# Optimization experiments

Measured on AMD Instinct MI355X. Metric: run time of the kernel, lower is better.

The kernel has to match this reference:

```python
import jax, jax.numpy as jnp
import numpy as np

T = 2048
HIDDEN = 4096
NH = 32        # query heads
NKV = 8        # kv heads
G = NH // NKV  # GQA group size
D = 128        # head_dim (== v_head_dim)
ROPE_BASE = 1000000.0


def setup_inputs() -> dict:
    key = jax.random.key(0)
    ks = jax.random.split(key, 8)
    s = 0.02
    return {
        "positions": jnp.arange(T, dtype=jnp.int32),
        "hidden_states": jax.random.normal(ks[0], (T, HIDDEN), dtype=jnp.float32),
        "Wq": jax.random.normal(ks[1], (HIDDEN, NH * D), dtype=jnp.float32) * s,
        "bq": jnp.zeros((NH * D,), dtype=jnp.float32),
        "Wk": jax.random.normal(ks[2], (HIDDEN, NKV * D), dtype=jnp.float32) * s,
        "bk": jnp.zeros((NKV * D,), dtype=jnp.float32),
        "Wv": jax.random.normal(ks[3], (HIDDEN, NKV * D), dtype=jnp.float32) * s,
        "bv": jnp.zeros((NKV * D,), dtype=jnp.float32),
        "Wo": jax.random.normal(ks[4], (NH * D, HIDDEN), dtype=jnp.float32) * s,
    }


def _rope(positions, x):
    # neox-style rotary, full rotary_dim = D
    half = D // 2
    inv_freq = 1.0 / (ROPE_BASE ** (jnp.arange(0, half, dtype=jnp.float32) / half))
    freqs = positions.astype(jnp.float32)[:, None] * inv_freq[None, :]  # [T, half]
    cos = jnp.cos(freqs)[:, None, :]  # [T, 1, half]
    sin = jnp.sin(freqs)[:, None, :]
    x1, x2 = x[..., :half], x[..., half:]
    return jnp.concatenate([x1 * cos - x2 * sin, x2 * cos + x1 * sin], axis=-1)


def reference(positions, hidden_states, Wq, bq, Wk, bk, Wv, bv, Wo):
    q = (hidden_states @ Wq + bq).reshape(T, NH, D)
    k = (hidden_states @ Wk + bk).reshape(T, NKV, D)
    v = (hidden_states @ Wv + bv).reshape(T, NKV, D)
    q = _rope(positions, q)
    k = _rope(positions, k)

    scale = D ** -0.5
    qg = q.reshape(T, NKV, G, D)
    # scores: [NKV, G, T(query), S(key)]
    scores = jnp.einsum("tkgd,skd->kgts", qg, k) * scale
    causal = positions[:, None] >= positions[None, :]  # [T, S]
    scores = jnp.where(causal[None, None, :, :], scores, jnp.finfo(scores.dtype).min)
    probs = jax.nn.softmax(scores, axis=-1)
    attn = jnp.einsum("kgts,skd->tkgd", probs, v).reshape(T, NH * D)

    output = attn @ Wo
    kv_fused = jnp.stack([k, v], axis=0)  # [2, T, NKV, D]
    return output, kv_fused
```

## Files before the change

### kernel.cpp

```cpp
#include <hip/hip_runtime.h>
#include <stdint.h>

#define T_SEQ 2048
#define HIDDEN_DIM 4096
#define NH 32
#define NKV 8
#define HD 128
#define QKV_N 6144

typedef unsigned short u16;
typedef __attribute__((__ext_vector_type__(8))) __bf16 bf16x8;
typedef __attribute__((__ext_vector_type__(4))) float f32x4;

__device__ __forceinline__ float exp2_fast(float x) {
    return __builtin_amdgcn_exp2f(x);
}

__device__ __forceinline__ u16 f2bf(float f) {
    union { float f; unsigned u; } x; x.f = f;
    unsigned u = x.u;
    unsigned r = u + 0x7FFFu + ((u >> 16) & 1u);
    return (u16)(r >> 16);
}
__device__ __forceinline__ float bf2f(u16 h) {
    union { unsigned u; float f; } x; x.u = ((unsigned)h) << 16;
    return x.f;
}

__device__ __forceinline__ void gl_lds16(const u16* g, u16* l) {
    __builtin_amdgcn_global_load_lds((__attribute__((address_space(1))) void*)g,
                                     (__attribute__((address_space(3))) void*)l,
                                     16, 0, 0);
}

__global__ __launch_bounds__(256) void cast_f32_bf16(const float* __restrict__ in,
                                                     u16* __restrict__ out, int n4) {
    int i = blockIdx.x * 256 + threadIdx.x;
    if (i < n4) {
        float4 v = ((const float4*)in)[i];
        uint2 o;
        o.x = (unsigned)f2bf(v.x) | ((unsigned)f2bf(v.y) << 16);
        o.y = (unsigned)f2bf(v.z) | ((unsigned)f2bf(v.w) << 16);
        ((uint2*)out)[i] = o;
    }
}

__global__ __launch_bounds__(256) void transpose_cast(const float* __restrict__ W,
                                                      u16* __restrict__ Wt, int R, int C) {
    __shared__ float tile[32][33];
    int c0 = blockIdx.x * 32, r0 = blockIdx.y * 32;
    int tx = threadIdx.x & 31;
    int ty = threadIdx.x >> 5;
#pragma unroll
    for (int i = 0; i < 32; i += 8)
        tile[ty + i][tx] = W[(size_t)(r0 + ty + i) * C + c0 + tx];
    __syncthreads();
#pragma unroll
    for (int i = 0; i < 32; i += 8)
        Wt[(size_t)(c0 + ty + i) * R + r0 + tx] = f2bf(tile[tx][ty + i]);
}

__global__ __launch_bounds__(256) void concat_bias(const float* __restrict__ bq,
                                                   const float* __restrict__ bk,
                                                   const float* __restrict__ bv,
                                                   float* __restrict__ out) {
    int i = blockIdx.x * 256 + threadIdx.x;
    if (i < 4096) out[i] = bq[i];
    else if (i < 5120) out[i] = bk[i - 4096];
    else if (i < 6144) out[i] = bv[i - 5120];
}

template <int BF16_OUT, int HAS_BIAS>
__global__ __launch_bounds__(256) void gemm_bt(const u16* __restrict__ A,
                                               const u16* __restrict__ Bt,
                                               const float* __restrict__ bias,
                                               void* __restrict__ Cv,
                                               int M, int N, int K) {
    __shared__ alignas(16) u16 As[128 * 32];
    __shared__ alignas(16) u16 Bs[128 * 32];
    const int tid = threadIdx.x;
    const int wave = tid >> 6;
    const int lane = tid & 63;
    const int l15 = lane & 15;
    const int quad = lane >> 4;
    const int m0 = blockIdx.y * 128;
    const int n0 = blockIdx.x * 128;
    const int wm = (wave >> 1) * 64;
    const int wn = (wave & 1) * 64;

    f32x4 acc[4][4] = {};

    const u16* Ag = A + (size_t)(m0 + wave * 32 + (lane >> 2)) * K + (lane & 3) * 8;
    const u16* Bg = Bt + (size_t)(n0 + wave * 32 + (lane >> 2)) * K + (lane & 3) * 8;
    u16* Al = &As[wave * 32 * 32];
    u16* Bl = &Bs[wave * 32 * 32];

    for (int k0 = 0; k0 < K; k0 += 32) {
        __syncthreads();
        gl_lds16(Ag + k0, Al);
        gl_lds16(Ag + k0 + (size_t)16 * K, Al + 16 * 32);
        gl_lds16(Bg + k0, Bl);
        gl_lds16(Bg + k0 + (size_t)16 * K, Bl + 16 * 32);
        __syncthreads();
        bf16x8 af[4], bfr[4];
#pragma unroll
        for (int i = 0; i < 4; ++i)
            af[i] = *(const bf16x8*)&As[(wm + i * 16 + l15) * 32 + quad * 8];
#pragma unroll
        for (int i = 0; i < 4; ++i)
            bfr[i] = *(const bf16x8*)&Bs[(wn + i * 16 + l15) * 32 + quad * 8];
#pragma unroll
        for (int i = 0; i < 4; ++i)
#pragma unroll
            for (int j = 0; j < 4; ++j)
                acc[i][j] = __builtin_amdgcn_mfma_f32_16x16x32_bf16(af[i], bfr[j], acc[i][j], 0, 0, 0);
    }

#pragma unroll
    for (int i = 0; i < 4; ++i)
#pragma unroll
        for (int j = 0; j < 4; ++j)
#pragma unroll
            for (int r = 0; r < 4; ++r) {
                int row = m0 + wm + i * 16 + quad * 4 + r;
                int col = n0 + wn + j * 16 + l15;
                float v = acc[i][j][r];
                if (HAS_BIAS) v += bias[col];
                if (BF16_OUT) ((u16*)Cv)[(size_t)row * N + col] = f2bf(v);
                else ((float*)Cv)[(size_t)row * N + col] = v;
            }
}

__global__ __launch_bounds__(256) void rope_kernel(const int* __restrict__ positions,
                                                   const u16* __restrict__ qkv,
                                                   u16* __restrict__ qh,
                                                   u16* __restrict__ kh,
                                                   u16* __restrict__ vt,
                                                   float* __restrict__ kv_out) {
    const int t = blockIdx.x;
    const float pos = (float)positions[t];
    const size_t rowbase = (size_t)t * QKV_N;
    const float nlog = -13.815510557964274f / 64.f;
    const float KZ = 0.08838834764831845f * 1.4426950408889634f;
    for (int col = threadIdx.x; col < QKV_N; col += 256) {
        if (col < 4096) {
            int hh = col >> 7, d = col & 127, j = d & 63;
            float ang = pos * __expf((float)j * nlog);
            float cs = cosf(ang), sn = sinf(ang);
            size_t base = rowbase + (size_t)(col & ~127);
            float x1 = bf2f(qkv[base + j]);
            float x2 = bf2f(qkv[base + 64 + j]);
            float v = (d < 64) ? (x1 * cs - x2 * sn) : (x2 * cs + x1 * sn);
            qh[((size_t)hh * T_SEQ + t) * HD + d] = f2bf(v * KZ);
        } else if (col < 5120) {
            int lc = col - 4096, hh = lc >> 7, d = lc & 127, j = d & 63;
            float ang = pos * __expf((float)j * nlog);
            float cs = cosf(ang), sn = sinf(ang);
            size_t base = rowbase + 4096 + (size_t)hh * 128;
            float x1 = bf2f(qkv[base + j]);
            float x2 = bf2f(qkv[base + 64 + j]);
            float v = (d < 64) ? (x1 * cs - x2 * sn) : (x2 * cs + x1 * sn);
            kh[((size_t)hh * T_SEQ + t) * HD + d] = f2bf(v);
            kv_out[((size_t)t * NKV + hh) * HD + d] = v;
        } else {
            int lc = col - 5120, hh = lc >> 7, d = lc & 127;
            float v = bf2f(qkv[rowbase + 5120 + (size_t)hh * 128 + d]);
            vt[((size_t)hh * HD + d) * T_SEQ + t] = f2bf(v);
            kv_out[(((size_t)T_SEQ + t) * NKV + hh) * HD + d] = v;
        }
    }
}

#define KS_STRIDE 136
#define VS_STRIDE 72
#define PS_STRIDE 72

__global__ __launch_bounds__(256) void attn_kernel(const u16* __restrict__ Qh,
                                                   const u16* __restrict__ Kh,
                                                   const u16* __restrict__ Vt,
                                                   u16* __restrict__ attn_out) {
    __shared__ alignas(16) u16 Ks[64 * KS_STRIDE];
    __shared__ alignas(16) u16 Vs[128 * VS_STRIDE];
    __shared__ alignas(16) u16 Ps[4][32 * PS_STRIDE];

    const int h = blockIdx.y;
    const int qb = (gridDim.x - 1) - blockIdx.x;
    const int tid = threadIdx.x;
    const int wave = tid >> 6;
    const int lane = tid & 63;
    const int l15 = lane & 15;
    const int quad = lane >> 4;
    const int kvh = h >> 2;
    const int wrow0 = qb * 128 + wave * 32;

    const u16* Qp = Qh + ((size_t)h * T_SEQ + wrow0) * HD;
    const u16* Kp = Kh + (size_t)kvh * T_SEQ * HD;
    const u16* Vp = Vt + (size_t)kvh * HD * T_SEQ;

    bf16x8 aQ[2][4];
#pragma unroll
    for (int i = 0; i < 2; ++i)
#pragma unroll
        for (int kb = 0; kb < 4; ++kb)
            aQ[i][kb] = *(const bf16x8*)&Qp[(size_t)(i * 16 + l15) * HD + kb * 32 + quad * 8];

    bf16x8 ones;
#pragma unroll
    for (int z = 0; z < 8; ++z) ones[z] = (__bf16)1.0f;

    f32x4 acc[2][8] = {};
    f32x4 accl[2] = {};

    const int n_tiles = 2 * qb + 2;

    const int krow = tid >> 4;
    const int kcol = (tid & 15) * 8;
    const int vrow = tid >> 3;
    const int vcol = (tid & 7) * 8;

#pragma unroll 1
    for (int t = 0; t < n_tiles; ++t) {
        const int s0 = t * 64;
        __syncthreads();
#pragma unroll
        for (int rep = 0; rep < 4; ++rep) {
            int r = krow + rep * 16;
            *(uint4*)&Ks[r * KS_STRIDE + kcol] =
                *(const uint4*)&Kp[(size_t)(s0 + r) * HD + kcol];
        }
#pragma unroll
        for (int rep = 0; rep < 4; ++rep) {
            int d = vrow + rep * 32;
            *(uint4*)&Vs[d * VS_STRIDE + vcol] =
                *(const uint4*)&Vp[(size_t)d * T_SEQ + s0 + vcol];
        }
        __syncthreads();

        if (s0 <= wrow0 + 31) {
            f32x4 sc[2][4];
#pragma unroll
            for (int j = 0; j < 4; ++j) {
                f32x4 sa = {}, sb = {};
#pragma unroll
                for (int kb = 0; kb < 4; ++kb) {
                    bf16x8 bK = *(const bf16x8*)&Ks[(j * 16 + l15) * KS_STRIDE + kb * 32 + quad * 8];
                    sa = __builtin_amdgcn_mfma_f32_16x16x32_bf16(aQ[0][kb], bK, sa, 0, 0, 0);
                    sb = __builtin_amdgcn_mfma_f32_16x16x32_bf16(aQ[1][kb], bK, sb, 0, 0, 0);
                }
                sc[0][j] = sa;
                sc[1][j] = sb;
            }
#pragma unroll
            for (int i = 0; i < 2; ++i)
#pragma unroll
                for (int r = 0; r < 4; ++r) {
                    int t_idx = wrow0 + i * 16 + quad * 4 + r;
#pragma unroll
                    for (int j = 0; j < 4; ++j) {
                        int s_idx = s0 + j * 16 + l15;
                        float z = (s_idx > t_idx) ? -1e30f : sc[i][j][r];
                        float p = exp2_fast(z);
                        Ps[wave][(i * 16 + quad * 4 + r) * PS_STRIDE + j * 16 + l15] = f2bf(p);
                    }
                }
            bf16x8 aP[2][2];
#pragma unroll
            for (int i = 0; i < 2; ++i)
#pragma unroll
                for (int k2 = 0; k2 < 2; ++k2)
                    aP[i][k2] = *(const bf16x8*)&Ps[wave][(i * 16 + l15) * PS_STRIDE + k2 * 32 + quad * 8];
#pragma unroll
            for (int o = 0; o < 8; ++o) {
                bf16x8 bV0 = *(const bf16x8*)&Vs[(o * 16 + l15) * VS_STRIDE + quad * 8];
                bf16x8 bV1 = *(const bf16x8*)&Vs[(o * 16 + l15) * VS_STRIDE + 32 + quad * 8];
#pragma unroll
                for (int i = 0; i < 2; ++i) {
                    acc[i][o] = __builtin_amdgcn_mfma_f32_16x16x32_bf16(aP[i][0], bV0, acc[i][o], 0, 0, 0);
                    acc[i][o] = __builtin_amdgcn_mfma_f32_16x16x32_bf16(aP[i][1], bV1, acc[i][o], 0, 0, 0);
                }
            }
#pragma unroll
            for (int i = 0; i < 2; ++i) {
                accl[i] = __builtin_amdgcn_mfma_f32_16x16x32_bf16(aP[i][0], ones, accl[i], 0, 0, 0);
                accl[i] = __builtin_amdgcn_mfma_f32_16x16x32_bf16(aP[i][1], ones, accl[i], 0, 0, 0);
            }
        }
    }

#pragma unroll
    for (int i = 0; i < 2; ++i)
#pragma unroll
        for (int r = 0; r < 4; ++r) {
            float inv = 1.f / accl[i][r];
            int t_idx = wrow0 + i * 16 + quad * 4 + r;
#pragma unroll
            for (int o = 0; o < 8; ++o)
                attn_out[(size_t)t_idx * (NH * HD) + h * HD + o * 16 + l15] =
                    f2bf(acc[i][o][r] * inv);
        }
}

extern "C" void kernel_launch(void* const* d_in, const int* in_sizes, int n_in,
                              void* d_out, int out_size, void* d_ws, size_t ws_size,
                              hipStream_t stream) {
    const int* positions = (const int*)d_in[0];
    const float* hidden = (const float*)d_in[1];
    const float* Wq = (const float*)d_in[2];
    const float* bq = (const float*)d_in[3];
    const float* Wk = (const float*)d_in[4];
    const float* bk = (const float*)d_in[5];
    const float* Wv = (const float*)d_in[6];
    const float* bv = (const float*)d_in[7];
    const float* Wo = (const float*)d_in[8];

    char* ws = (char*)d_ws;
    u16* hs_bf   = (u16*)(ws + 0);
    u16* attnbuf = (u16*)(ws + 0);
    u16* wqkvT   = (u16*)(ws + 16777216);
    u16* woT     = (u16*)(ws + 16777216);
    u16* qkvbuf  = (u16*)(ws + 67108864);
    u16* qbuf    = (u16*)(ws + 92274688);
    u16* kbuf    = (u16*)(ws + 109051904);
    u16* vtbuf   = (u16*)(ws + 113246208);
    float* biasb = (float*)(ws + 117440512);

    float* out0 = (float*)d_out;
    float* kvout = out0 + (size_t)T_SEQ * HIDDEN_DIM;

    cast_f32_bf16<<<dim3((T_SEQ * HIDDEN_DIM / 4 + 255) / 256), dim3(256), 0, stream>>>(
        hidden, hs_bf, T_SEQ * HIDDEN_DIM / 4);
    transpose_cast<<<dim3(128, 128), dim3(256), 0, stream>>>(Wq, wqkvT, HIDDEN_DIM, 4096);
    transpose_cast<<<dim3(32, 128), dim3(256), 0, stream>>>(Wk, wqkvT + (size_t)4096 * HIDDEN_DIM, HIDDEN_DIM, 1024);
    transpose_cast<<<dim3(32, 128), dim3(256), 0, stream>>>(Wv, wqkvT + (size_t)5120 * HIDDEN_DIM, HIDDEN_DIM, 1024);
    concat_bias<<<dim3(24), dim3(256), 0, stream>>>(bq, bk, bv, biasb);

    gemm_bt<1, 1><<<dim3(QKV_N / 128, T_SEQ / 128), dim3(256), 0, stream>>>(
        hs_bf, wqkvT, biasb, qkvbuf, T_SEQ, QKV_N, HIDDEN_DIM);

    transpose_cast<<<dim3(128, 128), dim3(256), 0, stream>>>(Wo, woT, NH * HD, HIDDEN_DIM);

    rope_kernel<<<dim3(T_SEQ), dim3(256), 0, stream>>>(positions, qkvbuf, qbuf, kbuf, vtbuf, kvout);

    attn_kernel<<<dim3(16, NH), dim3(256), 0, stream>>>(qbuf, kbuf, vtbuf, attnbuf);

    gemm_bt<0, 0><<<dim3(HIDDEN_DIM / 128, T_SEQ / 128), dim3(256), 0, stream>>>(
        attnbuf, woT, nullptr, out0, T_SEQ, HIDDEN_DIM, NH * HD);
}
```

Measured before the change: 580.2 us.

## Use 256x256-tile 4-stage pipelined GEMM for QKV projection

Adds a new 512-thread GEMM kernel with 256x256 output tiles, a 4-slot LDS ring buffer fed by direct global-to-LDS loads, XOR-swizzled LDS layout, setprio around MFMA bursts, and a blockIdx swizzle for L2 locality. It replaces the 128x128 QKV projection GEMM. The aim is more data reuse per tile and overlap of loads with MFMA. The cost is much higher register and LDS pressure (128 KB of LDS per block) and fewer blocks (192) on a large CU count, which may leave parts of the GPU underused.

```diff
diff --git a/kernel.cpp b/kernel.cpp
--- a/kernel.cpp
+++ b/kernel.cpp
@@ -32,6 +32,13 @@
                                      (__attribute__((address_space(3))) void*)l,
                                      16, 0, 0);
 }
+
+#define BAR()                                  \
+    {                                          \
+        asm volatile("" ::: "memory");         \
+        __builtin_amdgcn_s_barrier();          \
+        asm volatile("" ::: "memory");         \
+    }
 
 __global__ __launch_bounds__(256) void cast_f32_bf16(const float* __restrict__ in,
                                                      u16* __restrict__ out, int n4) {
@@ -129,6 +136,131 @@
                 if (BF16_OUT) ((u16*)Cv)[(size_t)row * N + col] = f2bf(v);
                 else ((float*)Cv)[(size_t)row * N + col] = v;
             }
+}
+
+#define KSTEP(S, SLOT, STG, VMW)                                                            \
+    {                                                                                       \
+        bf16x8 bf0_[4], af_[4];                                                             \
+        _Pragma("unroll") for (int n = 0; n < 4; ++n)                                       \
+            bf0_[n] = *(const bf16x8*)&Bs[SLOT][boff[n]];                                   \
+        _Pragma("unroll") for (int m = 0; m < 4; ++m)                                       \
+            af_[m] = *(const bf16x8*)&As[SLOT][aoff[m]];                                    \
+        if (STG) {                                                                          \
+            gl_lds16(Ast + (size_t)((S) + 3) * 32, &As[((SLOT) + 3) & 3][ldsS0]);           \
+            gl_lds16(Ast + (size_t)((S) + 3) * 32 + rowK128, &As[((SLOT) + 3) & 3][ldsS1]); \
+        }                                                                                   \
+        BAR();                                                                              \
+        __builtin_amdgcn_s_setprio(1);                                                      \
+        _Pragma("unroll") for (int m = 0; m < 4; ++m)                                       \
+            _Pragma("unroll") for (int n = 0; n < 4; ++n)                                   \
+                acc[m][n] = __builtin_amdgcn_mfma_f32_16x16x32_bf16(af_[m], bf0_[n],        \
+                                                                    acc[m][n], 0, 0, 0);    \
+        __builtin_amdgcn_s_setprio(0);                                                      \
+        BAR();                                                                              \
+        _Pragma("unroll") for (int m = 0; m < 4; ++m)                                       \
+            af_[m] = *(const bf16x8*)&As[SLOT][aoff[4 + m]];                                \
+        if (STG) {                                                                          \
+            gl_lds16(Bst + (size_t)((S) + 3) * 32, &Bs[((SLOT) + 3) & 3][ldsS0]);           \
+            gl_lds16(Bst + (size_t)((S) + 3) * 32 + rowK128, &Bs[((SLOT) + 3) & 3][ldsS1]); \
+        }                                                                                   \
+        BAR();                                                                              \
+        __builtin_amdgcn_s_setprio(1);                                                      \
+        _Pragma("unroll") for (int m = 0; m < 4; ++m)                                       \
+            _Pragma("unroll") for (int n = 0; n < 4; ++n)                                   \
+                acc[4 + m][n] = __builtin_amdgcn_mfma_f32_16x16x32_bf16(af_[m], bf0_[n],    \
+                                                                        acc[4 + m][n],      \
+                                                                        0, 0, 0);           \
+        __builtin_amdgcn_s_setprio(0);                                                      \
+        asm volatile("s_waitcnt vmcnt(" #VMW ")" ::: "memory");                             \
+        BAR();                                                                              \
+    }
+
+template <int BF16_OUT, int HAS_BIAS>
+__global__ __launch_bounds__(512, 2) void gemm256(const u16* __restrict__ A,
+                                                  const u16* __restrict__ Bt,
+                                                  const float* __restrict__ bias,
+                                                  void* __restrict__ Cv,
+                                                  int M, int N, int K) {
+    __shared__ alignas(16) u16 As[4][256 * 32];
+    __shared__ alignas(16) u16 Bs[4][256 * 32];
+    const int tid = threadIdx.x;
+    const int wave = tid >> 6;
+    const int lane = tid & 63;
+    const int l15 = lane & 15;
+    const int quad = lane >> 4;
+    const int wr = wave >> 2;
+    const int wc = wave & 3;
+
+    const int nbx = N >> 8;
+    const int q8 = (int)gridDim.x >> 3;
+    const int wg = blockIdx.x;
+    const int swz = (wg & 7) * q8 + (wg >> 3);
+    const int m0 = (swz / nbx) * 256;
+    const int n0 = (swz % nbx) * 256;
+
+    const int srow = tid >> 2;
+    const int schunk = (tid & 3) ^ ((tid >> 3) & 3);
+    const u16* Ast = A + (size_t)(m0 + srow) * K + schunk * 8;
+    const u16* Bst = Bt + (size_t)(n0 + srow) * K + schunk * 8;
+    const size_t rowK128 = (size_t)128 * K;
+    const int ldsS0 = wave * 512;
+    const int ldsS1 = 4096 + wave * 512;
+
+    int aoff[8], boff[4];
+#pragma unroll
+    for (int m = 0; m < 8; ++m) {
+        int row = wr * 128 + m * 16 + l15;
+        aoff[m] = row * 32 + ((quad ^ ((row >> 1) & 3)) << 3);
+    }
+#pragma unroll
+    for (int n = 0; n < 4; ++n) {
+        int row = wc * 64 + n * 16 + l15;
+        boff[n] = row * 32 + ((quad ^ ((row >> 1) & 3)) << 3);
+    }
+
+    f32x4 acc[8][4] = {};
+    const int NS = K >> 5;
+
+#pragma unroll
+    for (int s = 0; s < 3; ++s) {
+        gl_lds16(Ast + (size_t)s * 32, &As[s][ldsS0]);
+        gl_lds16(Ast + (size_t)s * 32 + rowK128, &As[s][ldsS1]);
+        gl_lds16(Bst + (size_t)s * 32, &Bs[s][ldsS0]);
+        gl_lds16(Bst + (size_t)s * 32 + rowK128, &Bs[s][ldsS1]);
+    }
+    asm volatile("s_waitcnt vmcnt(8)" ::: "memory");
+    BAR();
+
+#pragma unroll 1
+    for (int s = 0; s < NS - 4; s += 4) {
+        KSTEP(s, 0, 1, 4)
+        KSTEP(s + 1, 1, 1, 4)
+        KSTEP(s + 2, 2, 1, 4)
+        KSTEP(s + 3, 3, 1, 4)
+    }
+    {
+        const int s = NS - 4;
+        KSTEP(s, 0, 1, 4)
+        KSTEP(s + 1, 1, 0, 4)
+        KSTEP(s + 2, 2, 0, 0)
+        KSTEP(s + 3, 3, 0, 0)
+    }
+
+#pragma unroll
+    for (int m = 0; m < 8; ++m) {
+        const int row = m0 + wr * 128 + m * 16 + quad * 4;
+#pragma unroll
+        for (int n = 0; n < 4; ++n) {
+            const int col = n0 + wc * 64 + n * 16 + l15;
+            float b = HAS_BIAS ? bias[col] : 0.f;
+#pragma unroll
+            for (int r = 0; r < 4; ++r) {
+                float v = acc[m][n][r] + b;
+                if (BF16_OUT) ((u16*)Cv)[(size_t)(row + r) * N + col] = f2bf(v);
+                else ((float*)Cv)[(size_t)(row + r) * N + col] = v;
+            }
+        }
+    }
 }
 
 __global__ __launch_bounds__(256) void rope_kernel(const int* __restrict__ positions,
@@ -334,7 +466,7 @@
     transpose_cast<<<dim3(32, 128), dim3(256), 0, stream>>>(Wv, wqkvT + (size_t)5120 * HIDDEN_DIM, HIDDEN_DIM, 1024);
     concat_bias<<<dim3(24), dim3(256), 0, stream>>>(bq, bk, bv, biasb);
 
-    gemm_bt<1, 1><<<dim3(QKV_N / 128, T_SEQ / 128), dim3(256), 0, stream>>>(
+    gemm256<1, 1><<<dim3((T_SEQ / 256) * (QKV_N / 256)), dim3(512), 0, stream>>>(
         hs_bf, wqkvT, biasb, qkvbuf, T_SEQ, QKV_N, HIDDEN_DIM);
 
     transpose_cast<<<dim3(128, 128), dim3(256), 0, stream>>>(Wo, woT, NH * HD, HIDDEN_DIM);
```

Measured after the change: 564.2 us. 1.03x faster.

## Replace GEMMs with 4-stage pipelined, swizzled 512-thread MFMA kernel; zigzag attention schedule

Applied to the files above, without the earlier changes.

Replaces the single-buffered 128x128 GEMM with a templated kernel that uses a 4-slot LDS ring filled by global_load_lds. It double-buffers register fragments, waits on explicit vmcnt counts, swizzles LDS chunks against bank conflicts, remaps workgroups for L2 locality, and raises MFMA priority with s_setprio. The QKV and output projections get larger 256x192 and 128x256 tiles with 8 waves. Attention blocks are reordered in a zigzag pattern that alternates by head to balance causal work. The aim is to hide global-load latency and raise MFMA utilisation, at the cost of more LDS and registers per block and hand-tuned wait counts that must match the number of outstanding loads.

```diff
diff --git a/kernel.cpp b/kernel.cpp
--- a/kernel.cpp
+++ b/kernel.cpp
@@ -31,6 +31,22 @@
     __builtin_amdgcn_global_load_lds((__attribute__((address_space(1))) void*)g,
                                      (__attribute__((address_space(3))) void*)l,
                                      16, 0, 0);
+}
+
+#define BAR()                                  \
+    {                                          \
+        asm volatile("" ::: "memory");         \
+        __builtin_amdgcn_s_barrier();          \
+        asm volatile("" ::: "memory");         \
+    }
+
+template <int N>
+__device__ __forceinline__ void vmwait() {
+    if constexpr (N == 0) asm volatile("s_waitcnt vmcnt(0)" ::: "memory");
+    else if constexpr (N == 3) asm volatile("s_waitcnt vmcnt(3)" ::: "memory");
+    else if constexpr (N == 4) asm volatile("s_waitcnt vmcnt(4)" ::: "memory");
+    else if constexpr (N == 6) asm volatile("s_waitcnt vmcnt(6)" ::: "memory");
+    else if constexpr (N == 8) asm volatile("s_waitcnt vmcnt(8)" ::: "memory");
 }
 
 __global__ __launch_bounds__(256) void cast_f32_bf16(const float* __restrict__ in,
@@ -70,65 +86,128 @@
     else if (i < 6144) out[i] = bv[i - 5120];
 }
 
-template <int BF16_OUT, int HAS_BIAS>
-__global__ __launch_bounds__(256) void gemm_bt(const u16* __restrict__ A,
-                                               const u16* __restrict__ Bt,
-                                               const float* __restrict__ bias,
-                                               void* __restrict__ Cv,
-                                               int M, int N, int K) {
-    __shared__ alignas(16) u16 As[128 * 32];
-    __shared__ alignas(16) u16 Bs[128 * 32];
+#define STAGE(SL, S)                                                                         \
+    {                                                                                        \
+        const size_t ko_ = (size_t)(S) * 32;                                                 \
+        _Pragma("unroll") for (int c_ = 0; c_ < ACALLS; ++c_)                                \
+            gl_lds16(Ast + ko_ + (size_t)(c_ * 128) * K, &As[SL][c_ * 4096 + wave * 512]);   \
+        _Pragma("unroll") for (int c_ = 0; c_ < BFULL; ++c_)                                 \
+            gl_lds16(Bst + ko_ + (size_t)(c_ * 128) * K, &Bs[SL][c_ * 4096 + wave * 512]);   \
+        if (BHALF) gl_lds16(BstH + ko_, &Bs[SL][BFULL * 4096 + (wave & 3) * 512]);           \
+    }
+
+#define REGION(SLOT, NSLOT, CA, CB, NA, NB, RN)                                              \
+    {                                                                                        \
+        if (RN) {                                                                            \
+            _Pragma("unroll") for (int n_ = 0; n_ < NF; ++n_)                                \
+                NB[n_] = *(const bf16x8*)&Bs[NSLOT][boff[n_]];                               \
+            _Pragma("unroll") for (int m_ = 0; m_ < MF; ++m_)                                \
+                NA[m_] = *(const bf16x8*)&As[NSLOT][aoff[m_]];                               \
+        }                                                                                    \
+        __builtin_amdgcn_s_setprio(1);                                                       \
+        _Pragma("unroll") for (int m_ = 0; m_ < MF; ++m_)                                    \
+            _Pragma("unroll") for (int n_ = 0; n_ < NF; ++n_)                                \
+                acc[m_][n_] = __builtin_amdgcn_mfma_f32_16x16x32_bf16(CA[m_], CB[n_],        \
+                                                                      acc[m_][n_], 0, 0, 0); \
+        __builtin_amdgcn_s_setprio(0);                                                       \
+    }
+
+#define KSTEP(S, SLOT, STG, VMW, RN, CA, CB, NA, NB)          \
+    {                                                         \
+        if (STG) STAGE((((SLOT) + 3) & 3), (S) + 3)           \
+        vmwait<VMW>();                                        \
+        BAR();                                                \
+        REGION(SLOT, (((SLOT) + 1) & 3), CA, CB, NA, NB, RN)  \
+        BAR();                                                \
+    }
+
+template <int MF, int NF, int ACALLS, int BFULL, int BHALF, int BF16_OUT, int HAS_BIAS>
+__global__ __launch_bounds__(512, 2) void gemm_ph(const u16* __restrict__ A,
+                                                  const u16* __restrict__ Bt,
+                                                  const float* __restrict__ bias,
+                                                  void* __restrict__ Cv,
+                                                  int M, int N, int K) {
+    constexpr int BM = MF * 32;
+    constexpr int BN = NF * 64;
+    constexpr int LPS = ACALLS + BFULL + BHALF;
+    __shared__ alignas(16) u16 As[4][BM * 32];
+    __shared__ alignas(16) u16 Bs[4][BN * 32];
     const int tid = threadIdx.x;
     const int wave = tid >> 6;
     const int lane = tid & 63;
     const int l15 = lane & 15;
     const int quad = lane >> 4;
-    const int m0 = blockIdx.y * 128;
-    const int n0 = blockIdx.x * 128;
-    const int wm = (wave >> 1) * 64;
-    const int wn = (wave & 1) * 64;
-
-    f32x4 acc[4][4] = {};
-
-    const u16* Ag = A + (size_t)(m0 + wave * 32 + (lane >> 2)) * K + (lane & 3) * 8;
-    const u16* Bg = Bt + (size_t)(n0 + wave * 32 + (lane >> 2)) * K + (lane & 3) * 8;
-    u16* Al = &As[wave * 32 * 32];
-    u16* Bl = &Bs[wave * 32 * 32];
-
-    for (int k0 = 0; k0 < K; k0 += 32) {
-        __syncthreads();
-        gl_lds16(Ag + k0, Al);
-        gl_lds16(Ag + k0 + (size_t)16 * K, Al + 16 * 32);
-        gl_lds16(Bg + k0, Bl);
-        gl_lds16(Bg + k0 + (size_t)16 * K, Bl + 16 * 32);
-        __syncthreads();
-        bf16x8 af[4], bfr[4];
-#pragma unroll
-        for (int i = 0; i < 4; ++i)
-            af[i] = *(const bf16x8*)&As[(wm + i * 16 + l15) * 32 + quad * 8];
-#pragma unroll
-        for (int i = 0; i < 4; ++i)
-            bfr[i] = *(const bf16x8*)&Bs[(wn + i * 16 + l15) * 32 + quad * 8];
-#pragma unroll
-        for (int i = 0; i < 4; ++i)
-#pragma unroll
-            for (int j = 0; j < 4; ++j)
-                acc[i][j] = __builtin_amdgcn_mfma_f32_16x16x32_bf16(af[i], bfr[j], acc[i][j], 0, 0, 0);
-    }
-
-#pragma unroll
-    for (int i = 0; i < 4; ++i)
-#pragma unroll
-        for (int j = 0; j < 4; ++j)
+    const int wr = wave >> 2;
+    const int wc = wave & 3;
+
+    const int nbn = N / BN;
+    const int q8 = (int)gridDim.x >> 3;
+    const int wg = blockIdx.x;
+    const int swz = (wg & 7) * q8 + (wg >> 3);
+    const int m0 = (swz / nbn) * BM;
+    const int n0 = (swz % nbn) * BN;
+
+    const int srow = tid >> 2;
+    const int schunk = (tid & 3) ^ ((tid >> 3) & 3);
+    const u16* Ast = A + (size_t)(m0 + srow) * K + schunk * 8;
+    const u16* Bst = Bt + (size_t)(n0 + srow) * K + schunk * 8;
+    const int srowH = (tid & 255) >> 2;
+    const u16* BstH = Bt + (size_t)(n0 + BFULL * 128 + srowH) * K + schunk * 8;
+
+    int aoff[MF], boff[NF];
+#pragma unroll
+    for (int m = 0; m < MF; ++m) {
+        int row = wr * (MF * 16) + m * 16 + l15;
+        aoff[m] = row * 32 + ((quad ^ ((row >> 1) & 3)) << 3);
+    }
+#pragma unroll
+    for (int n = 0; n < NF; ++n) {
+        int row = wc * (NF * 16) + n * 16 + l15;
+        boff[n] = row * 32 + ((quad ^ ((row >> 1) & 3)) << 3);
+    }
+
+    bf16x8 fA0[MF], fB0[NF], fA1[MF], fB1[NF];
+    f32x4 acc[MF][NF] = {};
+    const int NS = K >> 5;
+
+    STAGE(0, 0) STAGE(1, 1) STAGE(2, 2)
+    vmwait<LPS>();
+    BAR();
+#pragma unroll
+    for (int n = 0; n < NF; ++n) fB0[n] = *(const bf16x8*)&Bs[0][boff[n]];
+#pragma unroll
+    for (int m = 0; m < MF; ++m) fA0[m] = *(const bf16x8*)&As[0][aoff[m]];
+
+#pragma unroll 1
+    for (int s = 0; s < NS - 4; s += 4) {
+        KSTEP(s, 0, 1, 2 * LPS, 1, fA0, fB0, fA1, fB1)
+        KSTEP(s + 1, 1, 1, 2 * LPS, 1, fA1, fB1, fA0, fB0)
+        KSTEP(s + 2, 2, 1, 2 * LPS, 1, fA0, fB0, fA1, fB1)
+        KSTEP(s + 3, 3, 1, 2 * LPS, 1, fA1, fB1, fA0, fB0)
+    }
+    {
+        const int s = NS - 4;
+        KSTEP(s, 0, 1, 2 * LPS, 1, fA0, fB0, fA1, fB1)
+        KSTEP(s + 1, 1, 0, LPS, 1, fA1, fB1, fA0, fB0)
+        KSTEP(s + 2, 2, 0, 0, 1, fA0, fB0, fA1, fB1)
+        KSTEP(s + 3, 3, 0, 0, 0, fA1, fB1, fA0, fB0)
+    }
+
+#pragma unroll
+    for (int m = 0; m < MF; ++m) {
+        const int row = m0 + wr * (MF * 16) + m * 16 + quad * 4;
+#pragma unroll
+        for (int n = 0; n < NF; ++n) {
+            const int col = n0 + wc * (NF * 16) + n * 16 + l15;
+            float b = HAS_BIAS ? bias[col] : 0.f;
 #pragma unroll
             for (int r = 0; r < 4; ++r) {
-                int row = m0 + wm + i * 16 + quad * 4 + r;
-                int col = n0 + wn + j * 16 + l15;
-                float v = acc[i][j][r];
-                if (HAS_BIAS) v += bias[col];
-                if (BF16_OUT) ((u16*)Cv)[(size_t)row * N + col] = f2bf(v);
-                else ((float*)Cv)[(size_t)row * N + col] = v;
+                float v = acc[m][n][r] + b;
+                if (BF16_OUT) ((u16*)Cv)[(size_t)(row + r) * N + col] = f2bf(v);
+                else ((float*)Cv)[(size_t)(row + r) * N + col] = v;
             }
+        }
+    }
 }
 
 __global__ __launch_bounds__(256) void rope_kernel(const int* __restrict__ positions,
@@ -184,7 +263,9 @@
     __shared__ alignas(16) u16 Ps[4][32 * PS_STRIDE];
 
     const int h = blockIdx.y;
-    const int qb = (gridDim.x - 1) - blockIdx.x;
+    const int x = blockIdx.x;
+    const int zig = (x & 1) ? ((x - 1) >> 1) : (15 - (x >> 1));
+    const int qb = (h < 16) ? zig : (15 - zig);
     const int tid = threadIdx.x;
     const int wave = tid >> 6;
     const int lane = tid & 63;
@@ -334,7 +415,7 @@
     transpose_cast<<<dim3(32, 128), dim3(256), 0, stream>>>(Wv, wqkvT + (size_t)5120 * HIDDEN_DIM, HIDDEN_DIM, 1024);
     concat_bias<<<dim3(24), dim3(256), 0, stream>>>(bq, bk, bv, biasb);
 
-    gemm_bt<1, 1><<<dim3(QKV_N / 128, T_SEQ / 128), dim3(256), 0, stream>>>(
+    gemm_ph<8, 3, 2, 1, 1, 1, 1><<<dim3((T_SEQ / 256) * (QKV_N / 192)), dim3(512), 0, stream>>>(
         hs_bf, wqkvT, biasb, qkvbuf, T_SEQ, QKV_N, HIDDEN_DIM);
 
     transpose_cast<<<dim3(128, 128), dim3(256), 0, stream>>>(Wo, woT, NH * HD, HIDDEN_DIM);
@@ -343,6 +424,6 @@
 
     attn_kernel<<<dim3(16, NH), dim3(256), 0, stream>>>(qbuf, kbuf, vtbuf, attnbuf);
 
-    gemm_bt<0, 0><<<dim3(HIDDEN_DIM / 128, T_SEQ / 128), dim3(256), 0, stream>>>(
+    gemm_ph<4, 4, 1, 2, 0, 0, 0><<<dim3((T_SEQ / 128) * (HIDDEN_DIM / 256)), dim3(512), 0, stream>>>(
         attnbuf, woT, nullptr, out0, T_SEQ, HIDDEN_DIM, NH * HD);
 }
```

After: 539.7 us. 1.07x faster.
